# Optimization experiments

Hardware: AMD Instinct MI355X
Metric: run time of the kernel (lower is better)

Reference implementation:

```python
import jax, jax.numpy as jnp
import numpy as np

E = 500_000
NODE_DIM = 128
EDGE_DIM = 128
GLOB_DIM = 64
NUM_GRAPHS = 64
HIDDEN = 4 * EDGE_DIM  # 512
IN_DIM = 2 * NODE_DIM + EDGE_DIM + GLOB_DIM  # 448
EPS = 1e-5


def setup_inputs() -> dict:
    key = jax.random.key(0)
    ks = jax.random.split(key, 12)
    src = jax.random.normal(ks[0], (E, NODE_DIM), dtype=jnp.float32)
    dest = jax.random.normal(ks[1], (E, NODE_DIM), dtype=jnp.float32)
    edge_attr = jax.random.normal(ks[2], (E, EDGE_DIM), dtype=jnp.float32)
    u = jax.random.normal(ks[3], (NUM_GRAPHS, GLOB_DIM), dtype=jnp.float32)
    batch = jnp.sort(jax.random.randint(ks[4], (E,), 0, NUM_GRAPHS, dtype=jnp.int32))
    # MLP params (kaiming-ish scale)
    W1 = jax.random.normal(ks[5], (IN_DIM, HIDDEN), dtype=jnp.float32) / np.sqrt(IN_DIM)
    b1 = jnp.zeros((HIDDEN,), dtype=jnp.float32)
    W2 = jax.random.normal(ks[6], (HIDDEN, EDGE_DIM), dtype=jnp.float32) / np.sqrt(HIDDEN)
    b2 = jnp.zeros((EDGE_DIM,), dtype=jnp.float32)
    # GraphNorm params
    gn_weight = jnp.ones((EDGE_DIM,), dtype=jnp.float32)
    gn_bias = jnp.zeros((EDGE_DIM,), dtype=jnp.float32)
    mean_scale = jnp.ones((EDGE_DIM,), dtype=jnp.float32)
    return {"src": src, "dest": dest, "edge_attr": edge_attr, "u": u, "batch": batch,
            "W1": W1, "b1": b1, "W2": W2, "b2": b2,
            "gn_weight": gn_weight, "gn_bias": gn_bias, "mean_scale": mean_scale}


def _graph_norm(x, batch, weight, bias, mean_scale):
    # per-graph mean
    cnt = jax.ops.segment_sum(jnp.ones((x.shape[0],), x.dtype), batch, num_segments=NUM_GRAPHS)
    cnt = jnp.maximum(cnt, 1.0)[:, None]  # [G,1]
    mean = jax.ops.segment_sum(x, batch, num_segments=NUM_GRAPHS) / cnt  # [G,D]
    out = x - mean[batch] * mean_scale
    var = jax.ops.segment_sum(out * out, batch, num_segments=NUM_GRAPHS) / cnt  # [G,D]
    std = jnp.sqrt(var + EPS)
    return out / std[batch] * weight + bias


def reference(src, dest, edge_attr, u, batch, W1, b1, W2, b2, gn_weight, gn_bias, mean_scale):
    # gather per-graph globals + concat: [E, 2*node+edge+glob]
    h = jnp.concatenate([src, dest, edge_attr, u[batch]], axis=1)
    h = jax.nn.relu(h @ W1 + b1) @ W2 + b2  # [E, edge_dim]
    out = _graph_norm(h + edge_attr, batch, gn_weight, gn_bias, mean_scale)
    return out  # dropout is identity in eval / p=0.0
```

## Files before the change

### kernel.cpp

```cpp
#include <hip/hip_runtime.h>
#include <stdint.h>

#define E_EDGES   500000
#define MBLK      32
#define NBLK      15625
#define EPSV      1e-5f

typedef unsigned short u16;
typedef __attribute__((ext_vector_type(8))) short short8;
typedef __attribute__((ext_vector_type(4))) float f32x4;

__device__ __forceinline__ u16 f2bf(float f) {
  uint32_t u = __float_as_uint(f);
  u += 0x7fffu + ((u >> 16) & 1u);
  return (u16)(u >> 16);
}

__global__ void prep_weights(const float* __restrict__ W1, const float* __restrict__ W2,
                             u16* __restrict__ w1f, u16* __restrict__ w2f) {
  int idx = blockIdx.x * blockDim.x + threadIdx.x;
  if (idx < 32*14*64) {
    int lane = idx & 63; int t = idx >> 6; int k32 = t % 14; int n16 = t / 14;
    int n = n16*16 + (lane & 15); int k0 = k32*32 + (lane >> 4)*8;
    short8 pk;
#pragma unroll
    for (int j = 0; j < 8; ++j) pk[j] = (short)f2bf(W1[(size_t)(k0 + j)*512 + n]);
    *(short8*)&w1f[(size_t)idx * 8] = pk;
  } else if (idx < 32*14*64 + 8*16*64) {
    int i2 = idx - 32*14*64;
    int lane = i2 & 63; int t = i2 >> 6; int k32 = t % 16; int n16 = t / 16;
    int n = n16*16 + (lane & 15); int k0 = k32*32 + (lane >> 4)*8;
    short8 pk;
#pragma unroll
    for (int j = 0; j < 8; ++j) pk[j] = (short)f2bf(W2[(size_t)(k0 + j)*128 + n]);
    *(short8*)&w2f[(size_t)i2 * 8] = pk;
  }
}

#define SWZ16(row, byte) ((byte) ^ (((row) & 7) << 4))

__global__ __launch_bounds__(256, 4)
void fused_kernel(const float* __restrict__ srcp, const float* __restrict__ destp,
                  const float* __restrict__ edgep, const float* __restrict__ up,
                  const int* __restrict__ batch, const float* __restrict__ b1,
                  const float* __restrict__ b2,
                  const u16* __restrict__ w1f, const u16* __restrict__ w2f,
                  float* __restrict__ outp,
                  float* __restrict__ sums0, float* __restrict__ sums2,
                  float* __restrict__ cntsh, int nshard) {
  const int tid  = threadIdx.x;
  const int lane = tid & 63;
  const int w    = tid >> 6;
  const int l15  = lane & 15, l4 = lane >> 4;

  __shared__ __align__(16) u16 lds[32*512];
  char* ldsb = (char*)lds;

  const long grow0 = (long)blockIdx.x * MBLK;

  {
    const int srow = tid >> 3;
    const int c8   = (tid & 7) * 8;
    const long sgrow = grow0 + srow;
    const int  bat = batch[sgrow];
#pragma unroll
    for (int j = 0; j < 7; ++j) {
      const float* sp;
      if (j == 0)      sp = srcp  + sgrow*128 + c8;
      else if (j == 1) sp = srcp  + sgrow*128 + 64 + c8;
      else if (j == 2) sp = destp + sgrow*128 + c8;
      else if (j == 3) sp = destp + sgrow*128 + 64 + c8;
      else if (j == 4) sp = edgep + sgrow*128 + c8;
      else if (j == 5) sp = edgep + sgrow*128 + 64 + c8;
      else             sp = up + (size_t)bat*64 + c8;
      f32x4 t0 = *(const f32x4*)(sp);
      f32x4 t1 = *(const f32x4*)(sp + 4);
      short8 pk;
      pk[0]=(short)f2bf(t0[0]); pk[1]=(short)f2bf(t0[1]);
      pk[2]=(short)f2bf(t0[2]); pk[3]=(short)f2bf(t0[3]);
      pk[4]=(short)f2bf(t1[0]); pk[5]=(short)f2bf(t1[1]);
      pk[6]=(short)f2bf(t1[2]); pk[7]=(short)f2bf(t1[3]);
      *(short8*)(ldsb + srow*896 + SWZ16(srow, (j*64 + c8)*2)) = pk;
    }
  }
  __syncthreads();

  f32x4 acc1[2][8];
#pragma unroll
  for (int mi = 0; mi < 2; ++mi)
#pragma unroll
    for (int nj = 0; nj < 8; ++nj) {
      float bv = b1[w*128 + nj*16 + l15];
      acc1[mi][nj] = (f32x4){bv, bv, bv, bv};
    }

#pragma unroll 2
  for (int k32 = 0; k32 < 14; ++k32) {
    short8 a[2], b[8];
#pragma unroll
    for (int mi = 0; mi < 2; ++mi) {
      int row = mi*16 + l15;
      a[mi] = *(const short8*)(ldsb + row*896 + SWZ16(row, k32*64 + l4*16));
    }
#pragma unroll
    for (int nj = 0; nj < 8; ++nj) {
      int n16 = w*8 + nj;
      b[nj] = *(const short8*)&w1f[((size_t)(n16*14 + k32)*64 + lane)*8];
    }
#pragma unroll
    for (int mi = 0; mi < 2; ++mi)
#pragma unroll
      for (int nj = 0; nj < 8; ++nj)
        acc1[mi][nj] = __builtin_amdgcn_mfma_f32_16x16x32_bf16(a[mi], b[nj], acc1[mi][nj], 0, 0, 0);
  }
  __syncthreads();

#pragma unroll
  for (int nj = 0; nj < 8; ++nj) {
    int n = w*128 + nj*16 + l15;
#pragma unroll
    for (int mi = 0; mi < 2; ++mi)
#pragma unroll
      for (int rr = 0; rr < 4; ++rr) {
        int row = mi*16 + l4*4 + rr;
        *(u16*)(ldsb + row*1024 + SWZ16(row, n*2)) = f2bf(fmaxf(acc1[mi][nj][rr], 0.f));
      }
  }
  __syncthreads();

  const int c4    = tid & 31;
  const int rbase = tid >> 5;
  f32x4 ebuf[4];
#pragma unroll
  for (int p = 0; p < 4; ++p)
    ebuf[p] = *(const f32x4*)(edgep + (grow0 + rbase + p*8)*128 + c4*4);

  f32x4 acc2[2][2];
#pragma unroll
  for (int nj = 0; nj < 2; ++nj) {
    float bv = b2[w*32 + nj*16 + l15];
    acc2[0][nj] = (f32x4){bv, bv, bv, bv};
    acc2[1][nj] = (f32x4){bv, bv, bv, bv};
  }

#pragma unroll 4
  for (int kb = 0; kb < 16; ++kb) {
    short8 a2[2], bf[2];
#pragma unroll
    for (int mi = 0; mi < 2; ++mi) {
      int row = mi*16 + l15;
      a2[mi] = *(const short8*)(ldsb + row*1024 + SWZ16(row, kb*64 + l4*16));
    }
#pragma unroll
    for (int nj = 0; nj < 2; ++nj) {
      int n16 = w*2 + nj;
      bf[nj] = *(const short8*)&w2f[(((size_t)(n16*16 + kb))*64 + lane)*8];
    }
#pragma unroll
    for (int mi = 0; mi < 2; ++mi)
#pragma unroll
      for (int nj = 0; nj < 2; ++nj)
        acc2[mi][nj] = __builtin_amdgcn_mfma_f32_16x16x32_bf16(a2[mi], bf[nj], acc2[mi][nj], 0, 0, 0);
  }
  __syncthreads();

#pragma unroll
  for (int mi = 0; mi < 2; ++mi)
#pragma unroll
    for (int nj = 0; nj < 2; ++nj) {
      int col = w*32 + nj*16 + l15;
#pragma unroll
      for (int rr = 0; rr < 4; ++rr) {
        int row = mi*16 + l4*4 + rr;
        *(float*)(ldsb + row*512 + SWZ16(row, col*4)) = acc2[mi][nj][rr];
      }
    }
  __syncthreads();

  const int g0 = batch[grow0];
  const int g1 = batch[grow0 + MBLK - 1];
  const int sh = blockIdx.x & (nshard - 1);

  if (g0 == g1) {
    f32x4 s = (f32x4){0,0,0,0}, s2 = (f32x4){0,0,0,0};
#pragma unroll
    for (int p = 0; p < 4; ++p) {
      int row = rbase + p*8;
      f32x4 y = *(const f32x4*)(ldsb + row*512 + SWZ16(row, c4*16));
      y = y + ebuf[p];
      *(f32x4*)(outp + (grow0 + row)*128 + c4*4) = y;
      s = s + y; s2 = s2 + y*y;
    }
    int slot = 16384 + (rbase*32 + c4)*32;
    *(f32x4*)(ldsb + slot)      = s;
    *(f32x4*)(ldsb + slot + 16) = s2;
    __syncthreads();
    int c4r = tid >> 3, stat = (tid >> 2) & 1, cq = tid & 3;
    float v = 0.f;
#pragma unroll
    for (int r = 0; r < 8; ++r)
      v += *(const float*)(ldsb + 16384 + (r*32 + c4r)*32 + stat*16 + cq*4);
    float* dst = stat ? sums2 : sums0;
    atomicAdd(&dst[(size_t)sh*8192 + g0*128 + c4r*4 + cq], v);
    if (tid == 0) atomicAdd(&cntsh[sh*64 + g0], (float)MBLK);
  } else {
    f32x4 s = (f32x4){0,0,0,0}, s2 = (f32x4){0,0,0,0};
    float rc = 0.f; int gcur = -1;
#pragma unroll
    for (int p = 0; p < 4; ++p) {
      int row = rbase + p*8;
      int g = batch[grow0 + row];
      if (g != gcur) {
        if (gcur >= 0) {
#pragma unroll
          for (int c = 0; c < 4; ++c) {
            atomicAdd(&sums0[(size_t)sh*8192 + gcur*128 + c4*4 + c], s[c]);
            atomicAdd(&sums2[(size_t)sh*8192 + gcur*128 + c4*4 + c], s2[c]);
          }
          if (c4 == 0) atomicAdd(&cntsh[sh*64 + gcur], rc);
        }
        gcur = g; s = (f32x4){0,0,0,0}; s2 = (f32x4){0,0,0,0}; rc = 0.f;
      }
      f32x4 y = *(const f32x4*)(ldsb + row*512 + SWZ16(row, c4*16));
      y = y + ebuf[p];
      *(f32x4*)(outp + (grow0 + row)*128 + c4*4) = y;
      s = s + y; s2 = s2 + y*y; rc += 1.f;
    }
#pragma unroll
    for (int c = 0; c < 4; ++c) {
      atomicAdd(&sums0[(size_t)sh*8192 + gcur*128 + c4*4 + c], s[c]);
      atomicAdd(&sums2[(size_t)sh*8192 + gcur*128 + c4*4 + c], s2[c]);
    }
    if (c4 == 0) atomicAdd(&cntsh[sh*64 + gcur], rc);
  }
}

__global__ void finalize_kernel(const float* __restrict__ sums0, const float* __restrict__ sums2,
                                const float* __restrict__ cntsh, int nshard,
                                const float* __restrict__ gnw, const float* __restrict__ gnb,
                                const float* __restrict__ ms,
                                float* __restrict__ scale, float* __restrict__ shift) {
  int idx = blockIdx.x*blockDim.x + threadIdx.x;
  if (idx >= 64*128) return;
  int g = idx >> 7, d = idx & 127;
  float s = 0.f, s2 = 0.f, c = 0.f;
  for (int sh = 0; sh < nshard; ++sh) {
    s  += sums0[(size_t)sh*8192 + idx];
    s2 += sums2[(size_t)sh*8192 + idx];
    c  += cntsh[sh*64 + g];
  }
  c = fmaxf(c, 1.0f);
  float mean = s / c;
  float mm = mean * ms[d];
  float var = fmaxf(s2 / c - 2.f*mm*mean + mm*mm, 0.f);
  float sc = gnw[d] / sqrtf(var + EPSV);
  scale[idx] = sc;
  shift[idx] = gnb[d] - mm*sc;
}

__global__ void norm_kernel(float* __restrict__ y, const int* __restrict__ batch,
                            const float* __restrict__ scale, const float* __restrict__ shift) {
  long i = (long)blockIdx.x*blockDim.x + threadIdx.x;
  const long n4 = (long)E_EDGES * 32;
  long stride = (long)gridDim.x*blockDim.x;
  for (; i < n4; i += stride) {
    long row = i >> 5;
    int dq = (int)(i & 31) << 2;
    int g = batch[row];
    f32x4 v = *(f32x4*)(y + i*4);
    f32x4 sc = *(const f32x4*)(scale + g*128 + dq);
    f32x4 sh = *(const f32x4*)(shift + g*128 + dq);
    v = v*sc + sh;
    *(f32x4*)(y + i*4) = v;
  }
}

extern "C" void kernel_launch(void* const* d_in, const int* in_sizes, int n_in,
                              void* d_out, int out_size, void* d_ws, size_t ws_size,
                              hipStream_t stream) {
  const float* srcp  = (const float*)d_in[0];
  const float* destp = (const float*)d_in[1];
  const float* edgep = (const float*)d_in[2];
  const float* up    = (const float*)d_in[3];
  const int*   batch = (const int*)d_in[4];
  const float* W1    = (const float*)d_in[5];
  const float* b1    = (const float*)d_in[6];
  const float* W2    = (const float*)d_in[7];
  const float* b2    = (const float*)d_in[8];
  const float* gnw   = (const float*)d_in[9];
  const float* gnb   = (const float*)d_in[10];
  const float* ms    = (const float*)d_in[11];
  float* outp = (float*)d_out;

  char* ws = (char*)d_ws;
  u16*   w1f   = (u16*)(ws + 0);
  u16*   w2f   = (u16*)(ws + 458752);
  float* scale = (float*)(ws + 589824);
  float* shift = (float*)(ws + 622592);
  float* cntsh = (float*)(ws + 655360);
  int nshard = 32;
  while (nshard > 1 && 663552 + (size_t)nshard*65536 > ws_size) nshard >>= 1;
  float* sums0 = (float*)(ws + 663552);
  float* sums2 = (float*)(ws + 663552 + (size_t)nshard*32768);

  hipMemsetAsync(ws + 655360, 0, 8192 + (size_t)nshard*65536, stream);
  prep_weights<<<dim3(144), dim3(256), 0, stream>>>(W1, W2, w1f, w2f);

  fused_kernel<<<dim3(NBLK), dim3(256), 0, stream>>>(srcp, destp, edgep, up, batch,
                                                     b1, b2, w1f, w2f, outp,
                                                     sums0, sums2, cntsh, nshard);

  finalize_kernel<<<dim3(32), dim3(256), 0, stream>>>(sums0, sums2, cntsh, nshard,
                                                      gnw, gnb, ms, scale, shift);
  norm_kernel<<<dim3(2048), dim3(256), 0, stream>>>(outp, batch, scale, shift);
}
```

Before: 577.4 us.

## Double fused kernel block to 512 threads and split MFMA N-tiles across eight waves

The fused MLP kernel now launches 512 threads (8 waves) per 32-row block instead of 256, so each wave handles half as many N-tiles in both GEMMs and stages fewer elements per thread. The per-graph statistics reduction switches to cross-lane shuffles followed by an LDS combine, and boundary blocks now issue per-row atomics instead of run-length grouping. The bf16 conversion uses the library intrinsic. This aims to raise latency hiding and per-block parallelism, at the cost of more register pressure per CU under the new launch bounds and more atomics on mixed-graph blocks.

```diff
diff --git a/kernel.cpp b/kernel.cpp
--- a/kernel.cpp
+++ b/kernel.cpp
@@ -1,4 +1,5 @@
 #include <hip/hip_runtime.h>
+#include <hip/hip_bf16.h>
 #include <stdint.h>
 
 #define E_EDGES   500000
@@ -9,11 +10,14 @@
 typedef unsigned short u16;
 typedef __attribute__((ext_vector_type(8))) short short8;
 typedef __attribute__((ext_vector_type(4))) float f32x4;
+typedef __attribute__((ext_vector_type(2))) uint32_t u32x2;
 
 __device__ __forceinline__ u16 f2bf(float f) {
-  uint32_t u = __float_as_uint(f);
-  u += 0x7fffu + ((u >> 16) & 1u);
-  return (u16)(u >> 16);
+  __hip_bfloat16 h = __float2bfloat16(f);
+  return *(u16*)&h;
+}
+__device__ __forceinline__ uint32_t pk2bf(float lo, float hi) {
+  return (uint32_t)f2bf(lo) | ((uint32_t)f2bf(hi) << 16);
 }
 
 __global__ void prep_weights(const float* __restrict__ W1, const float* __restrict__ W2,
@@ -39,7 +43,7 @@
 
 #define SWZ16(row, byte) ((byte) ^ (((row) & 7) << 4))
 
-__global__ __launch_bounds__(256, 4)
+__global__ __launch_bounds__(512, 4)
 void fused_kernel(const float* __restrict__ srcp, const float* __restrict__ destp,
                   const float* __restrict__ edgep, const float* __restrict__ up,
                   const int* __restrict__ batch, const float* __restrict__ b1,
@@ -58,66 +62,59 @@
 
   const long grow0 = (long)blockIdx.x * MBLK;
 
-  {
-    const int srow = tid >> 3;
-    const int c8   = (tid & 7) * 8;
-    const long sgrow = grow0 + srow;
-    const int  bat = batch[sgrow];
-#pragma unroll
-    for (int j = 0; j < 7; ++j) {
-      const float* sp;
-      if (j == 0)      sp = srcp  + sgrow*128 + c8;
-      else if (j == 1) sp = srcp  + sgrow*128 + 64 + c8;
-      else if (j == 2) sp = destp + sgrow*128 + c8;
-      else if (j == 3) sp = destp + sgrow*128 + 64 + c8;
-      else if (j == 4) sp = edgep + sgrow*128 + c8;
-      else if (j == 5) sp = edgep + sgrow*128 + 64 + c8;
-      else             sp = up + (size_t)bat*64 + c8;
-      f32x4 t0 = *(const f32x4*)(sp);
-      f32x4 t1 = *(const f32x4*)(sp + 4);
-      short8 pk;
-      pk[0]=(short)f2bf(t0[0]); pk[1]=(short)f2bf(t0[1]);
-      pk[2]=(short)f2bf(t0[2]); pk[3]=(short)f2bf(t0[3]);
-      pk[4]=(short)f2bf(t1[0]); pk[5]=(short)f2bf(t1[1]);
-      pk[6]=(short)f2bf(t1[2]); pk[7]=(short)f2bf(t1[3]);
-      *(short8*)(ldsb + srow*896 + SWZ16(srow, (j*64 + c8)*2)) = pk;
-    }
-  }
-  __syncthreads();
-
-  f32x4 acc1[2][8];
-#pragma unroll
-  for (int mi = 0; mi < 2; ++mi)
-#pragma unroll
-    for (int nj = 0; nj < 8; ++nj) {
-      float bv = b1[w*128 + nj*16 + l15];
-      acc1[mi][nj] = (f32x4){bv, bv, bv, bv};
-    }
+  const int srow = tid >> 4;
+  const int sq   = tid & 15;
+  const long sgrow = grow0 + srow;
+  const int bat = batch[sgrow];
+
+#pragma unroll
+  for (int j = 0; j < 7; ++j) {
+    const float* sp;
+    if (j == 0)      sp = srcp  + sgrow*128 + sq*4;
+    else if (j == 1) sp = srcp  + sgrow*128 + 64 + sq*4;
+    else if (j == 2) sp = destp + sgrow*128 + sq*4;
+    else if (j == 3) sp = destp + sgrow*128 + 64 + sq*4;
+    else if (j == 4) sp = edgep + sgrow*128 + sq*4;
+    else if (j == 5) sp = edgep + sgrow*128 + 64 + sq*4;
+    else             sp = up + (size_t)bat*64 + sq*4;
+    f32x4 t = *(const f32x4*)sp;
+    u32x2 pk = (u32x2){pk2bf(t[0], t[1]), pk2bf(t[2], t[3])};
+    *(u32x2*)(ldsb + srow*896 + SWZ16(srow, (j*64 + sq*4)*2)) = pk;
+  }
+  __syncthreads();
+
+  f32x4 acc1[2][4];
+#pragma unroll
+  for (int nj = 0; nj < 4; ++nj) {
+    float bv = b1[(w*4 + nj)*16 + l15];
+    acc1[0][nj] = (f32x4){bv, bv, bv, bv};
+    acc1[1][nj] = (f32x4){bv, bv, bv, bv};
+  }
 
 #pragma unroll 2
   for (int k32 = 0; k32 < 14; ++k32) {
-    short8 a[2], b[8];
+    short8 a[2], b[4];
 #pragma unroll
     for (int mi = 0; mi < 2; ++mi) {
       int row = mi*16 + l15;
       a[mi] = *(const short8*)(ldsb + row*896 + SWZ16(row, k32*64 + l4*16));
     }
 #pragma unroll
-    for (int nj = 0; nj < 8; ++nj) {
-      int n16 = w*8 + nj;
+    for (int nj = 0; nj < 4; ++nj) {
+      int n16 = w*4 + nj;
       b[nj] = *(const short8*)&w1f[((size_t)(n16*14 + k32)*64 + lane)*8];
     }
 #pragma unroll
     for (int mi = 0; mi < 2; ++mi)
 #pragma unroll
-      for (int nj = 0; nj < 8; ++nj)
+      for (int nj = 0; nj < 4; ++nj)
         acc1[mi][nj] = __builtin_amdgcn_mfma_f32_16x16x32_bf16(a[mi], b[nj], acc1[mi][nj], 0, 0, 0);
   }
   __syncthreads();
 
 #pragma unroll
-  for (int nj = 0; nj < 8; ++nj) {
-    int n = w*128 + nj*16 + l15;
+  for (int nj = 0; nj < 4; ++nj) {
+    int n = (w*4 + nj)*16 + l15;
 #pragma unroll
     for (int mi = 0; mi < 2; ++mi)
 #pragma unroll
@@ -128,52 +125,36 @@
   }
   __syncthreads();
 
-  const int c4    = tid & 31;
-  const int rbase = tid >> 5;
-  f32x4 ebuf[4];
-#pragma unroll
-  for (int p = 0; p < 4; ++p)
-    ebuf[p] = *(const f32x4*)(edgep + (grow0 + rbase + p*8)*128 + c4*4);
-
-  f32x4 acc2[2][2];
-#pragma unroll
-  for (int nj = 0; nj < 2; ++nj) {
-    float bv = b2[w*32 + nj*16 + l15];
-    acc2[0][nj] = (f32x4){bv, bv, bv, bv};
-    acc2[1][nj] = (f32x4){bv, bv, bv, bv};
-  }
+  f32x4 ebuf0 = *(const f32x4*)(edgep + sgrow*128 + sq*4);
+  f32x4 ebuf1 = *(const f32x4*)(edgep + sgrow*128 + 64 + sq*4);
+
+  const int col = w*16 + l15;
+  float bv2 = b2[col];
+  f32x4 acc2[2];
+  acc2[0] = (f32x4){bv2, bv2, bv2, bv2};
+  acc2[1] = (f32x4){bv2, bv2, bv2, bv2};
 
 #pragma unroll 4
   for (int kb = 0; kb < 16; ++kb) {
-    short8 a2[2], bf[2];
+    short8 hb[2];
 #pragma unroll
     for (int mi = 0; mi < 2; ++mi) {
       int row = mi*16 + l15;
-      a2[mi] = *(const short8*)(ldsb + row*1024 + SWZ16(row, kb*64 + l4*16));
-    }
-#pragma unroll
-    for (int nj = 0; nj < 2; ++nj) {
-      int n16 = w*2 + nj;
-      bf[nj] = *(const short8*)&w2f[(((size_t)(n16*16 + kb))*64 + lane)*8];
-    }
+      hb[mi] = *(const short8*)(ldsb + row*1024 + SWZ16(row, kb*64 + l4*16));
+    }
+    short8 bfrag = *(const short8*)&w2f[((size_t)(w*16 + kb)*64 + lane)*8];
 #pragma unroll
     for (int mi = 0; mi < 2; ++mi)
-#pragma unroll
-      for (int nj = 0; nj < 2; ++nj)
-        acc2[mi][nj] = __builtin_amdgcn_mfma_f32_16x16x32_bf16(a2[mi], bf[nj], acc2[mi][nj], 0, 0, 0);
+      acc2[mi] = __builtin_amdgcn_mfma_f32_16x16x32_bf16(hb[mi], bfrag, acc2[mi], 0, 0, 0);
   }
   __syncthreads();
 
 #pragma unroll
   for (int mi = 0; mi < 2; ++mi)
 #pragma unroll
-    for (int nj = 0; nj < 2; ++nj) {
-      int col = w*32 + nj*16 + l15;
-#pragma unroll
-      for (int rr = 0; rr < 4; ++rr) {
-        int row = mi*16 + l4*4 + rr;
-        *(float*)(ldsb + row*512 + SWZ16(row, col*4)) = acc2[mi][nj][rr];
-      }
+    for (int rr = 0; rr < 4; ++rr) {
+      int m = mi*16 + l4*4 + rr;
+      *(float*)(ldsb + m*512 + SWZ16(m, col*4)) = acc2[mi][rr];
     }
   __syncthreads();
 
@@ -181,57 +162,54 @@
   const int g1 = batch[grow0 + MBLK - 1];
   const int sh = blockIdx.x & (nshard - 1);
 
+  f32x4 y0 = *(const f32x4*)(ldsb + srow*512 + SWZ16(srow, sq*16));
+  f32x4 y1 = *(const f32x4*)(ldsb + srow*512 + SWZ16(srow, sq*16 + 256));
+  y0 = y0 + ebuf0;
+  y1 = y1 + ebuf1;
+  *(f32x4*)(outp + sgrow*128 + sq*4)      = y0;
+  *(f32x4*)(outp + sgrow*128 + 64 + sq*4) = y1;
+
   if (g0 == g1) {
-    f32x4 s = (f32x4){0,0,0,0}, s2 = (f32x4){0,0,0,0};
-#pragma unroll
-    for (int p = 0; p < 4; ++p) {
-      int row = rbase + p*8;
-      f32x4 y = *(const f32x4*)(ldsb + row*512 + SWZ16(row, c4*16));
-      y = y + ebuf[p];
-      *(f32x4*)(outp + (grow0 + row)*128 + c4*4) = y;
-      s = s + y; s2 = s2 + y*y;
-    }
-    int slot = 16384 + (rbase*32 + c4)*32;
-    *(f32x4*)(ldsb + slot)      = s;
-    *(f32x4*)(ldsb + slot + 16) = s2;
+    f32x4 s0 = y0, s0q = y0*y0, s1 = y1, s1q = y1*y1;
+#pragma unroll
+    for (int m = 16; m <= 32; m <<= 1) {
+#pragma unroll
+      for (int c = 0; c < 4; ++c) {
+        s0[c]  += __shfl_xor(s0[c],  m);
+        s0q[c] += __shfl_xor(s0q[c], m);
+        s1[c]  += __shfl_xor(s1[c],  m);
+        s1q[c] += __shfl_xor(s1q[c], m);
+      }
+    }
+    if (l4 == 0) {
+      int slotA = 16384 + (w*32 + l15)*32;
+      int slotB = 16384 + (w*32 + l15 + 16)*32;
+      *(f32x4*)(ldsb + slotA)      = s0;
+      *(f32x4*)(ldsb + slotA + 16) = s0q;
+      *(f32x4*)(ldsb + slotB)      = s1;
+      *(f32x4*)(ldsb + slotB + 16) = s1q;
+    }
     __syncthreads();
-    int c4r = tid >> 3, stat = (tid >> 2) & 1, cq = tid & 3;
-    float v = 0.f;
-#pragma unroll
-    for (int r = 0; r < 8; ++r)
-      v += *(const float*)(ldsb + 16384 + (r*32 + c4r)*32 + stat*16 + cq*4);
-    float* dst = stat ? sums2 : sums0;
-    atomicAdd(&dst[(size_t)sh*8192 + g0*128 + c4r*4 + cq], v);
+    if (tid < 256) {
+      int q = tid >> 3, st = (tid >> 2) & 1, c = tid & 3;
+      float v = 0.f;
+#pragma unroll
+      for (int w8 = 0; w8 < 8; ++w8)
+        v += *(const float*)(ldsb + 16384 + (w8*32 + q)*32 + st*16 + c*4);
+      float* dst = st ? sums2 : sums0;
+      atomicAdd(&dst[(size_t)sh*8192 + g0*128 + q*4 + c], v);
+    }
     if (tid == 0) atomicAdd(&cntsh[sh*64 + g0], (float)MBLK);
   } else {
-    f32x4 s = (f32x4){0,0,0,0}, s2 = (f32x4){0,0,0,0};
-    float rc = 0.f; int gcur = -1;
-#pragma unroll
-    for (int p = 0; p < 4; ++p) {
-      int row = rbase + p*8;
-      int g = batch[grow0 + row];
-      if (g != gcur) {
-        if (gcur >= 0) {
-#pragma unroll
-          for (int c = 0; c < 4; ++c) {
-            atomicAdd(&sums0[(size_t)sh*8192 + gcur*128 + c4*4 + c], s[c]);
-            atomicAdd(&sums2[(size_t)sh*8192 + gcur*128 + c4*4 + c], s2[c]);
-          }
-          if (c4 == 0) atomicAdd(&cntsh[sh*64 + gcur], rc);
-        }
-        gcur = g; s = (f32x4){0,0,0,0}; s2 = (f32x4){0,0,0,0}; rc = 0.f;
-      }
-      f32x4 y = *(const f32x4*)(ldsb + row*512 + SWZ16(row, c4*16));
-      y = y + ebuf[p];
-      *(f32x4*)(outp + (grow0 + row)*128 + c4*4) = y;
-      s = s + y; s2 = s2 + y*y; rc += 1.f;
-    }
+    int g = bat;
 #pragma unroll
     for (int c = 0; c < 4; ++c) {
-      atomicAdd(&sums0[(size_t)sh*8192 + gcur*128 + c4*4 + c], s[c]);
-      atomicAdd(&sums2[(size_t)sh*8192 + gcur*128 + c4*4 + c], s2[c]);
-    }
-    if (c4 == 0) atomicAdd(&cntsh[sh*64 + gcur], rc);
+      atomicAdd(&sums0[(size_t)sh*8192 + g*128 + sq*4 + c],      y0[c]);
+      atomicAdd(&sums2[(size_t)sh*8192 + g*128 + sq*4 + c],      y0[c]*y0[c]);
+      atomicAdd(&sums0[(size_t)sh*8192 + g*128 + 64 + sq*4 + c], y1[c]);
+      atomicAdd(&sums2[(size_t)sh*8192 + g*128 + 64 + sq*4 + c], y1[c]*y1[c]);
+    }
+    if (sq == 0) atomicAdd(&cntsh[sh*64 + g], 1.0f);
   }
 }
 
@@ -306,7 +284,7 @@
   hipMemsetAsync(ws + 655360, 0, 8192 + (size_t)nshard*65536, stream);
   prep_weights<<<dim3(144), dim3(256), 0, stream>>>(W1, W2, w1f, w2f);
 
-  fused_kernel<<<dim3(NBLK), dim3(256), 0, stream>>>(srcp, destp, edgep, up, batch,
+  fused_kernel<<<dim3(NBLK), dim3(512), 0, stream>>>(srcp, destp, edgep, up, batch,
                                                      b1, b2, w1f, w2f, outp,
                                                      sums0, sums2, cntsh, nshard);
 
```

Result: slower. 632.9 us (+9.6%).

## Keep hidden activations in registers via transposed MFMA and split-K second GEMM

Applied to the files above, without the earlier changes.

Swaps MFMA operand order in the first GEMM so the hidden tile comes out transposed, then repacks it to bf16 with lane shuffles into A-fragments for the second GEMM. This removes the LDS round trip and two barriers for the 32x512 hidden tile. The second GEMM is split along K across the four waves, and partial sums are reduced with LDS float atomics into a zeroed buffer. Bias b2 is added in the epilogue. LDS grows to about 52KB and launch bounds drop to 3 blocks per SM, trading occupancy and LDS atomic contention for fewer barriers and less LDS traffic.

```diff
diff --git a/kernel.cpp b/kernel.cpp
--- a/kernel.cpp
+++ b/kernel.cpp
@@ -1,19 +1,25 @@
 #include <hip/hip_runtime.h>
+#include <hip/hip_bf16.h>
 #include <stdint.h>
 
 #define E_EDGES   500000
 #define MBLK      32
 #define NBLK      15625
 #define EPSV      1e-5f
+#define YOFF      28672
+#define STOFF     45056
 
 typedef unsigned short u16;
 typedef __attribute__((ext_vector_type(8))) short short8;
 typedef __attribute__((ext_vector_type(4))) float f32x4;
+typedef __attribute__((ext_vector_type(4))) uint32_t u32x4;
 
 __device__ __forceinline__ u16 f2bf(float f) {
-  uint32_t u = __float_as_uint(f);
-  u += 0x7fffu + ((u >> 16) & 1u);
-  return (u16)(u >> 16);
+  __hip_bfloat16 h = __float2bfloat16(f);
+  return *(u16*)&h;
+}
+__device__ __forceinline__ uint32_t pk2bf(float lo, float hi) {
+  return (uint32_t)f2bf(lo) | ((uint32_t)f2bf(hi) << 16);
 }
 
 __global__ void prep_weights(const float* __restrict__ W1, const float* __restrict__ W2,
@@ -39,11 +45,11 @@
 
 #define SWZ16(row, byte) ((byte) ^ (((row) & 7) << 4))
 
-__global__ __launch_bounds__(256, 4)
+__global__ __launch_bounds__(256, 3)
 void fused_kernel(const float* __restrict__ srcp, const float* __restrict__ destp,
                   const float* __restrict__ edgep, const float* __restrict__ up,
-                  const int* __restrict__ batch, const float* __restrict__ b1,
-                  const float* __restrict__ b2,
+                  const int* __restrict__ batch, const float* __restrict__ b1p,
+                  const float* __restrict__ b2p,
                   const u16* __restrict__ w1f, const u16* __restrict__ w2f,
                   float* __restrict__ outp,
                   float* __restrict__ sums0, float* __restrict__ sums2,
@@ -53,10 +59,15 @@
   const int w    = tid >> 6;
   const int l15  = lane & 15, l4 = lane >> 4;
 
-  __shared__ __align__(16) u16 lds[32*512];
-  char* ldsb = (char*)lds;
+  __shared__ __align__(16) char ldsb[53248];
 
   const long grow0 = (long)blockIdx.x * MBLK;
+
+  {
+    f32x4 z = (f32x4){0.f, 0.f, 0.f, 0.f};
+#pragma unroll
+    for (int q = 0; q < 4; ++q) *(f32x4*)(ldsb + YOFF + tid*64 + q*16) = z;
+  }
 
   {
     const int srow = tid >> 3;
@@ -87,46 +98,55 @@
 
   f32x4 acc1[2][8];
 #pragma unroll
-  for (int mi = 0; mi < 2; ++mi)
-#pragma unroll
-    for (int nj = 0; nj < 8; ++nj) {
-      float bv = b1[w*128 + nj*16 + l15];
-      acc1[mi][nj] = (f32x4){bv, bv, bv, bv};
-    }
+  for (int nj = 0; nj < 8; ++nj) {
+    f32x4 bv = *(const f32x4*)&b1p[(w*8 + nj)*16 + l4*4];
+    acc1[0][nj] = bv;
+    acc1[1][nj] = bv;
+  }
 
 #pragma unroll 2
   for (int k32 = 0; k32 < 14; ++k32) {
-    short8 a[2], b[8];
+    short8 xb[2], wa[8];
 #pragma unroll
     for (int mi = 0; mi < 2; ++mi) {
       int row = mi*16 + l15;
-      a[mi] = *(const short8*)(ldsb + row*896 + SWZ16(row, k32*64 + l4*16));
-    }
-#pragma unroll
-    for (int nj = 0; nj < 8; ++nj) {
-      int n16 = w*8 + nj;
-      b[nj] = *(const short8*)&w1f[((size_t)(n16*14 + k32)*64 + lane)*8];
-    }
+      xb[mi] = *(const short8*)(ldsb + row*896 + SWZ16(row, k32*64 + l4*16));
+    }
+#pragma unroll
+    for (int nj = 0; nj < 8; ++nj)
+      wa[nj] = *(const short8*)&w1f[((size_t)((w*8 + nj)*14 + k32)*64 + lane)*8];
 #pragma unroll
     for (int mi = 0; mi < 2; ++mi)
 #pragma unroll
       for (int nj = 0; nj < 8; ++nj)
-        acc1[mi][nj] = __builtin_amdgcn_mfma_f32_16x16x32_bf16(a[mi], b[nj], acc1[mi][nj], 0, 0, 0);
-  }
-  __syncthreads();
-
-#pragma unroll
-  for (int nj = 0; nj < 8; ++nj) {
-    int n = w*128 + nj*16 + l15;
-#pragma unroll
-    for (int mi = 0; mi < 2; ++mi)
-#pragma unroll
-      for (int rr = 0; rr < 4; ++rr) {
-        int row = mi*16 + l4*4 + rr;
-        *(u16*)(ldsb + row*1024 + SWZ16(row, n*2)) = f2bf(fmaxf(acc1[mi][nj][rr], 0.f));
-      }
-  }
-  __syncthreads();
+        acc1[mi][nj] = __builtin_amdgcn_mfma_f32_16x16x32_bf16(wa[nj], xb[mi], acc1[mi][nj], 0, 0, 0);
+  }
+
+  const int src0 = l15 + (((l4 & 1) * 2) << 4);
+  const int src1 = src0 + 16;
+  const bool hsel = (l4 >> 1) != 0;
+  u32x4 hfrag[2][4];
+#pragma unroll
+  for (int mi = 0; mi < 2; ++mi)
+#pragma unroll
+    for (int kb = 0; kb < 4; ++kb) {
+      f32x4 vA = acc1[mi][kb*2];
+      f32x4 vB = acc1[mi][kb*2 + 1];
+      uint32_t pAlo = pk2bf(fmaxf(vA[0],0.f), fmaxf(vA[1],0.f));
+      uint32_t pAhi = pk2bf(fmaxf(vA[2],0.f), fmaxf(vA[3],0.f));
+      uint32_t pBlo = pk2bf(fmaxf(vB[0],0.f), fmaxf(vB[1],0.f));
+      uint32_t pBhi = pk2bf(fmaxf(vB[2],0.f), fmaxf(vB[3],0.f));
+      uint32_t a0 = (uint32_t)__shfl((int)pAlo, src0, 64);
+      uint32_t a1 = (uint32_t)__shfl((int)pAhi, src0, 64);
+      uint32_t a2 = (uint32_t)__shfl((int)pAlo, src1, 64);
+      uint32_t a3 = (uint32_t)__shfl((int)pAhi, src1, 64);
+      uint32_t c0 = (uint32_t)__shfl((int)pBlo, src0, 64);
+      uint32_t c1 = (uint32_t)__shfl((int)pBhi, src0, 64);
+      uint32_t c2 = (uint32_t)__shfl((int)pBlo, src1, 64);
+      uint32_t c3 = (uint32_t)__shfl((int)pBhi, src1, 64);
+      hfrag[mi][kb] = (u32x4){ hsel ? c0 : a0, hsel ? c1 : a1,
+                               hsel ? c2 : a2, hsel ? c3 : a3 };
+    }
 
   const int c4    = tid & 31;
   const int rbase = tid >> 5;
@@ -134,47 +154,39 @@
 #pragma unroll
   for (int p = 0; p < 4; ++p)
     ebuf[p] = *(const f32x4*)(edgep + (grow0 + rbase + p*8)*128 + c4*4);
-
-  f32x4 acc2[2][2];
-#pragma unroll
-  for (int nj = 0; nj < 2; ++nj) {
-    float bv = b2[w*32 + nj*16 + l15];
-    acc2[0][nj] = (f32x4){bv, bv, bv, bv};
-    acc2[1][nj] = (f32x4){bv, bv, bv, bv};
-  }
-
-#pragma unroll 4
-  for (int kb = 0; kb < 16; ++kb) {
-    short8 a2[2], bf[2];
-#pragma unroll
-    for (int mi = 0; mi < 2; ++mi) {
-      int row = mi*16 + l15;
-      a2[mi] = *(const short8*)(ldsb + row*1024 + SWZ16(row, kb*64 + l4*16));
-    }
-#pragma unroll
-    for (int nj = 0; nj < 2; ++nj) {
-      int n16 = w*2 + nj;
-      bf[nj] = *(const short8*)&w2f[(((size_t)(n16*16 + kb))*64 + lane)*8];
-    }
-#pragma unroll
-    for (int mi = 0; mi < 2; ++mi)
-#pragma unroll
-      for (int nj = 0; nj < 2; ++nj)
-        acc2[mi][nj] = __builtin_amdgcn_mfma_f32_16x16x32_bf16(a2[mi], bf[nj], acc2[mi][nj], 0, 0, 0);
-  }
-  __syncthreads();
-
+  f32x4 b2q = *(const f32x4*)&b2p[c4*4];
+
+  f32x4 acc2[2][8];
 #pragma unroll
   for (int mi = 0; mi < 2; ++mi)
 #pragma unroll
-    for (int nj = 0; nj < 2; ++nj) {
-      int col = w*32 + nj*16 + l15;
+    for (int njo = 0; njo < 8; ++njo)
+      acc2[mi][njo] = (f32x4){0.f, 0.f, 0.f, 0.f};
+
+#pragma unroll
+  for (int kb = 0; kb < 4; ++kb) {
+    short8 af[2];
+    af[0] = *(const short8*)&hfrag[0][kb];
+    af[1] = *(const short8*)&hfrag[1][kb];
+#pragma unroll
+    for (int njo = 0; njo < 8; ++njo) {
+      short8 wb = *(const short8*)&w2f[((size_t)(njo*16 + (w*4 + kb))*64 + lane)*8];
+#pragma unroll
+      for (int mi = 0; mi < 2; ++mi)
+        acc2[mi][njo] = __builtin_amdgcn_mfma_f32_16x16x32_bf16(af[mi], wb, acc2[mi][njo], 0, 0, 0);
+    }
+  }
+
+#pragma unroll
+  for (int mi = 0; mi < 2; ++mi)
+#pragma unroll
+    for (int njo = 0; njo < 8; ++njo)
 #pragma unroll
       for (int rr = 0; rr < 4; ++rr) {
-        int row = mi*16 + l4*4 + rr;
-        *(float*)(ldsb + row*512 + SWZ16(row, col*4)) = acc2[mi][nj][rr];
+        int m = mi*16 + l4*4 + rr;
+        int n = njo*16 + l15;
+        atomicAdd((float*)(ldsb + YOFF + m*512 + SWZ16(m, n*4)), acc2[mi][njo][rr]);
       }
-    }
   __syncthreads();
 
   const int g0 = batch[grow0];
@@ -186,12 +198,12 @@
 #pragma unroll
     for (int p = 0; p < 4; ++p) {
       int row = rbase + p*8;
-      f32x4 y = *(const f32x4*)(ldsb + row*512 + SWZ16(row, c4*16));
-      y = y + ebuf[p];
+      f32x4 y = *(const f32x4*)(ldsb + YOFF + row*512 + SWZ16(row, c4*16));
+      y = y + b2q + ebuf[p];
       *(f32x4*)(outp + (grow0 + row)*128 + c4*4) = y;
       s = s + y; s2 = s2 + y*y;
     }
-    int slot = 16384 + (rbase*32 + c4)*32;
+    int slot = STOFF + (rbase*32 + c4)*32;
     *(f32x4*)(ldsb + slot)      = s;
     *(f32x4*)(ldsb + slot + 16) = s2;
     __syncthreads();
@@ -199,7 +211,7 @@
     float v = 0.f;
 #pragma unroll
     for (int r = 0; r < 8; ++r)
-      v += *(const float*)(ldsb + 16384 + (r*32 + c4r)*32 + stat*16 + cq*4);
+      v += *(const float*)(ldsb + STOFF + (r*32 + c4r)*32 + stat*16 + cq*4);
     float* dst = stat ? sums2 : sums0;
     atomicAdd(&dst[(size_t)sh*8192 + g0*128 + c4r*4 + cq], v);
     if (tid == 0) atomicAdd(&cntsh[sh*64 + g0], (float)MBLK);
@@ -221,8 +233,8 @@
         }
         gcur = g; s = (f32x4){0,0,0,0}; s2 = (f32x4){0,0,0,0}; rc = 0.f;
       }
-      f32x4 y = *(const f32x4*)(ldsb + row*512 + SWZ16(row, c4*16));
-      y = y + ebuf[p];
+      f32x4 y = *(const f32x4*)(ldsb + YOFF + row*512 + SWZ16(row, c4*16));
+      y = y + b2q + ebuf[p];
       *(f32x4*)(outp + (grow0 + row)*128 + c4*4) = y;
       s = s + y; s2 = s2 + y*y; rc += 1.f;
     }
```

Result: slower. 1.563 ms (+170.7%).

## Double-buffer weight fragment loads in both GEMM loops and lower occupancy target

Applied to the files above, without the earlier changes.

Both MFMA k-loops now prefetch the next k-step's weight fragments from global memory into a second register buffer while the current step's MFMAs run, hiding global-load latency. The launch bounds drop from 4 to 3 blocks per SM to leave room for the extra registers. The float-to-bf16 conversion now uses the HIP intrinsic and the LDS stores are packed into two 8-byte writes. Lower occupancy may reduce latency hiding elsewhere, and the intrinsic may round NaN differently.

```diff
diff --git a/kernel.cpp b/kernel.cpp
--- a/kernel.cpp
+++ b/kernel.cpp
@@ -1,4 +1,5 @@
 #include <hip/hip_runtime.h>
+#include <hip/hip_bf16.h>
 #include <stdint.h>
 
 #define E_EDGES   500000
@@ -9,11 +10,14 @@
 typedef unsigned short u16;
 typedef __attribute__((ext_vector_type(8))) short short8;
 typedef __attribute__((ext_vector_type(4))) float f32x4;
+typedef __attribute__((ext_vector_type(2))) uint32_t u32x2;
 
 __device__ __forceinline__ u16 f2bf(float f) {
-  uint32_t u = __float_as_uint(f);
-  u += 0x7fffu + ((u >> 16) & 1u);
-  return (u16)(u >> 16);
+  __hip_bfloat16 h = __float2bfloat16(f);
+  return *(u16*)&h;
+}
+__device__ __forceinline__ uint32_t pk2bf(float lo, float hi) {
+  return (uint32_t)f2bf(lo) | ((uint32_t)f2bf(hi) << 16);
 }
 
 __global__ void prep_weights(const float* __restrict__ W1, const float* __restrict__ W2,
@@ -39,7 +43,7 @@
 
 #define SWZ16(row, byte) ((byte) ^ (((row) & 7) << 4))
 
-__global__ __launch_bounds__(256, 4)
+__global__ __launch_bounds__(256, 3)
 void fused_kernel(const float* __restrict__ srcp, const float* __restrict__ destp,
                   const float* __restrict__ edgep, const float* __restrict__ up,
                   const int* __restrict__ batch, const float* __restrict__ b1,
@@ -75,49 +79,73 @@
       else             sp = up + (size_t)bat*64 + c8;
       f32x4 t0 = *(const f32x4*)(sp);
       f32x4 t1 = *(const f32x4*)(sp + 4);
-      short8 pk;
-      pk[0]=(short)f2bf(t0[0]); pk[1]=(short)f2bf(t0[1]);
-      pk[2]=(short)f2bf(t0[2]); pk[3]=(short)f2bf(t0[3]);
-      pk[4]=(short)f2bf(t1[0]); pk[5]=(short)f2bf(t1[1]);
-      pk[6]=(short)f2bf(t1[2]); pk[7]=(short)f2bf(t1[3]);
-      *(short8*)(ldsb + srow*896 + SWZ16(srow, (j*64 + c8)*2)) = pk;
+      u32x2 lohi0 = (u32x2){pk2bf(t0[0], t0[1]), pk2bf(t0[2], t0[3])};
+      u32x2 lohi1 = (u32x2){pk2bf(t1[0], t1[1]), pk2bf(t1[2], t1[3])};
+      char* dst = ldsb + srow*896 + SWZ16(srow, (j*64 + c8)*2);
+      *(u32x2*)(dst)     = lohi0;
+      *(u32x2*)(dst + 8) = lohi1;
     }
   }
   __syncthreads();
 
   f32x4 acc1[2][8];
 #pragma unroll
-  for (int mi = 0; mi < 2; ++mi)
-#pragma unroll
-    for (int nj = 0; nj < 8; ++nj) {
-      float bv = b1[w*128 + nj*16 + l15];
-      acc1[mi][nj] = (f32x4){bv, bv, bv, bv};
-    }
-
-#pragma unroll 2
-  for (int k32 = 0; k32 < 14; ++k32) {
-    short8 a[2], b[8];
-#pragma unroll
-    for (int mi = 0; mi < 2; ++mi) {
-      int row = mi*16 + l15;
-      a[mi] = *(const short8*)(ldsb + row*896 + SWZ16(row, k32*64 + l4*16));
-    }
-#pragma unroll
-    for (int nj = 0; nj < 8; ++nj) {
-      int n16 = w*8 + nj;
-      b[nj] = *(const short8*)&w1f[((size_t)(n16*14 + k32)*64 + lane)*8];
-    }
-#pragma unroll
-    for (int mi = 0; mi < 2; ++mi)
+  for (int nj = 0; nj < 8; ++nj) {
+    float bv = b1[(w*8 + nj)*16 + l15];
+    acc1[0][nj] = (f32x4){bv, bv, bv, bv};
+    acc1[1][nj] = (f32x4){bv, bv, bv, bv};
+  }
+
+  {
+    short8 bA[8], bB[8];
+#pragma unroll
+    for (int nj = 0; nj < 8; ++nj)
+      bA[nj] = *(const short8*)&w1f[((size_t)((w*8 + nj)*14 + 0)*64 + lane)*8];
+
+#pragma unroll 1
+    for (int kk = 0; kk < 7; ++kk) {
+      int k32 = kk*2;
 #pragma unroll
       for (int nj = 0; nj < 8; ++nj)
-        acc1[mi][nj] = __builtin_amdgcn_mfma_f32_16x16x32_bf16(a[mi], b[nj], acc1[mi][nj], 0, 0, 0);
+        bB[nj] = *(const short8*)&w1f[((size_t)((w*8 + nj)*14 + (k32+1))*64 + lane)*8];
+      {
+        short8 a[2];
+#pragma unroll
+        for (int mi = 0; mi < 2; ++mi) {
+          int row = mi*16 + l15;
+          a[mi] = *(const short8*)(ldsb + row*896 + SWZ16(row, k32*64 + l4*16));
+        }
+#pragma unroll
+        for (int mi = 0; mi < 2; ++mi)
+#pragma unroll
+          for (int nj = 0; nj < 8; ++nj)
+            acc1[mi][nj] = __builtin_amdgcn_mfma_f32_16x16x32_bf16(a[mi], bA[nj], acc1[mi][nj], 0, 0, 0);
+      }
+      if (kk < 6) {
+#pragma unroll
+        for (int nj = 0; nj < 8; ++nj)
+          bA[nj] = *(const short8*)&w1f[((size_t)((w*8 + nj)*14 + (k32+2))*64 + lane)*8];
+      }
+      {
+        short8 a[2];
+#pragma unroll
+        for (int mi = 0; mi < 2; ++mi) {
+          int row = mi*16 + l15;
+          a[mi] = *(const short8*)(ldsb + row*896 + SWZ16(row, (k32+1)*64 + l4*16));
+        }
+#pragma unroll
+        for (int mi = 0; mi < 2; ++mi)
+#pragma unroll
+          for (int nj = 0; nj < 8; ++nj)
+            acc1[mi][nj] = __builtin_amdgcn_mfma_f32_16x16x32_bf16(a[mi], bB[nj], acc1[mi][nj], 0, 0, 0);
+      }
+    }
   }
   __syncthreads();
 
 #pragma unroll
   for (int nj = 0; nj < 8; ++nj) {
-    int n = w*128 + nj*16 + l15;
+    int n = (w*8 + nj)*16 + l15;
 #pragma unroll
     for (int mi = 0; mi < 2; ++mi)
 #pragma unroll
@@ -138,37 +166,63 @@
   f32x4 acc2[2][2];
 #pragma unroll
   for (int nj = 0; nj < 2; ++nj) {
-    float bv = b2[w*32 + nj*16 + l15];
+    float bv = b2[(w*2 + nj)*16 + l15];
     acc2[0][nj] = (f32x4){bv, bv, bv, bv};
     acc2[1][nj] = (f32x4){bv, bv, bv, bv};
   }
 
-#pragma unroll 4
-  for (int kb = 0; kb < 16; ++kb) {
-    short8 a2[2], bf[2];
-#pragma unroll
-    for (int mi = 0; mi < 2; ++mi) {
-      int row = mi*16 + l15;
-      a2[mi] = *(const short8*)(ldsb + row*1024 + SWZ16(row, kb*64 + l4*16));
-    }
+  {
+    short8 wA[2], wB[2];
+#pragma unroll
+    for (int nj = 0; nj < 2; ++nj)
+      wA[nj] = *(const short8*)&w2f[(((size_t)((w*2 + nj)*16 + 0))*64 + lane)*8];
+
+#pragma unroll 1
+    for (int kkb = 0; kkb < 8; ++kkb) {
+      int kb = kkb*2;
+#pragma unroll
+      for (int nj = 0; nj < 2; ++nj)
+        wB[nj] = *(const short8*)&w2f[(((size_t)((w*2 + nj)*16 + (kb+1)))*64 + lane)*8];
+      {
+        short8 hb[2];
+#pragma unroll
+        for (int mi = 0; mi < 2; ++mi) {
+          int row = mi*16 + l15;
+          hb[mi] = *(const short8*)(ldsb + row*1024 + SWZ16(row, kb*64 + l4*16));
+        }
+#pragma unroll
+        for (int mi = 0; mi < 2; ++mi)
+#pragma unroll
+          for (int nj = 0; nj < 2; ++nj)
+            acc2[mi][nj] = __builtin_amdgcn_mfma_f32_16x16x32_bf16(hb[mi], wA[nj], acc2[mi][nj], 0, 0, 0);
+      }
+      if (kkb < 7) {
+#pragma unroll
+        for (int nj = 0; nj < 2; ++nj)
+          wA[nj] = *(const short8*)&w2f[(((size_t)((w*2 + nj)*16 + (kb+2)))*64 + lane)*8];
+      }
+      {
+        short8 hb[2];
+#pragma unroll
+        for (int mi = 0; mi < 2; ++mi) {
+          int row = mi*16 + l15;
+          hb[mi] = *(const short8*)(ldsb + row*1024 + SWZ16(row, (kb+1)*64 + l4*16));
+        }
+#pragma unroll
+        for (int mi = 0; mi < 2; ++mi)
+#pragma unroll
+          for (int nj = 0; nj < 2; ++nj)
+            acc2[mi][nj] = __builtin_amdgcn_mfma_f32_16x16x32_bf16(hb[mi], wB[nj], acc2[mi][nj], 0, 0, 0);
+      }
+    }
+  }
+  __syncthreads();
+
+#pragma unroll
+  for (int mi = 0; mi < 2; ++mi)
 #pragma unroll
     for (int nj = 0; nj < 2; ++nj) {
-      int n16 = w*2 + nj;
-      bf[nj] = *(const short8*)&w2f[(((size_t)(n16*16 + kb))*64 + lane)*8];
-    }
-#pragma unroll
-    for (int mi = 0; mi < 2; ++mi)
-#pragma unroll
-      for (int nj = 0; nj < 2; ++nj)
-        acc2[mi][nj] = __builtin_amdgcn_mfma_f32_16x16x32_bf16(a2[mi], bf[nj], acc2[mi][nj], 0, 0, 0);
-  }
-  __syncthreads();
-
-#pragma unroll
-  for (int mi = 0; mi < 2; ++mi)
-#pragma unroll
-    for (int nj = 0; nj < 2; ++nj) {
-      int col = w*32 + nj*16 + l15;
+      int col = (w*2 + nj)*16 + l15;
 #pragma unroll
       for (int rr = 0; rr < 4; ++rr) {
         int row = mi*16 + l4*4 + rr;
```

New measurement: 569.5 us, median of 3. About the same (-1.4%).
